# Performance work log

Measured on AMD Instinct MI355X. Metric: run time of the kernel, lower is better.

The kernel has to match this reference:

```python
import jax, jax.numpy as jnp
import numpy as np

N = 50000          # nodes
E = 1_600_000      # edges
H = 64             # agg_hidden (heads=1, concat)
IN = 7             # in_channels
EDIM = 4           # edge_dim
G = 256            # num graphs in batch
FC = 128           # fc_hidden
NC = 2             # num_classes
SLOPE = 0.2        # GATv2 LeakyReLU negative slope


def setup_inputs() -> dict:
    key = jax.random.key(0)
    ks = jax.random.split(key, 24)
    s = 0.1
    d = {
        "x": jax.random.normal(ks[0], (N, IN), dtype=jnp.float32),
        "edge_index": jax.random.randint(ks[1], (2, E), 0, N, dtype=jnp.int32),
        "edge_attr": jax.random.normal(ks[2], (E, EDIM), dtype=jnp.float32),
        "batch": jnp.sort(jax.random.randint(ks[3], (N,), 0, G, dtype=jnp.int32)),
        # GATv2 layer 0 (in=7 -> 64)
        "Wl0": jax.random.normal(ks[4], (IN, H)) * s,
        "bl0": jnp.zeros((H,), jnp.float32),
        "Wr0": jax.random.normal(ks[5], (IN, H)) * s,
        "br0": jnp.zeros((H,), jnp.float32),
        "We0": jax.random.normal(ks[6], (EDIM, H)) * s,
        "att0": jax.random.normal(ks[7], (H,)) * s,
        "bias0": jnp.zeros((H,), jnp.float32),
        # GATv2 layer 1 (64 -> 64)
        "Wl1": jax.random.normal(ks[8], (H, H)) * s,
        "bl1": jnp.zeros((H,), jnp.float32),
        "Wr1": jax.random.normal(ks[9], (H, H)) * s,
        "br1": jnp.zeros((H,), jnp.float32),
        "We1": jax.random.normal(ks[10], (EDIM, H)) * s,
        "att1": jax.random.normal(ks[11], (H,)) * s,
        "bias1": jnp.zeros((H,), jnp.float32),
        # MLP head
        "fc1_w": jax.random.normal(ks[12], (H, FC)) * s,
        "fc1_b": jnp.zeros((FC,), jnp.float32),
        "fc2_w": jax.random.normal(ks[13], (FC, NC)) * s,
        "fc2_b": jnp.zeros((NC,), jnp.float32),
    }
    return d


def _gatv2(x, src, dst, edge_attr, Wl, bl, Wr, br, We, att, bias):
    # GATv2Conv (heads=1, concat=True, edge_dim=EDIM), eval mode (no dropout)
    xl = x @ Wl + bl                         # source-side projection [N,H]
    xr = x @ Wr + br                         # target-side projection [N,H]
    e = xl[src] + xr[dst] + edge_attr @ We   # per-edge pre-activation [E,H]
    score = jax.nn.leaky_relu(e, SLOPE) @ att  # [E]
    # segment softmax over destination nodes
    m = jax.ops.segment_max(score, dst, num_segments=N)
    ex = jnp.exp(score - m[dst])
    den = jax.ops.segment_sum(ex, dst, num_segments=N)
    alpha = ex / (den[dst] + 1e-16)
    out = jax.ops.segment_sum(xl[src] * alpha[:, None], dst, num_segments=N)
    return out + bias


def reference(x, edge_index, edge_attr, batch,
              Wl0, bl0, Wr0, br0, We0, att0, bias0,
              Wl1, bl1, Wr1, br1, We1, att1, bias1,
              fc1_w, fc1_b, fc2_w, fc2_b):
    src, dst = edge_index[0], edge_index[1]
    h = jax.nn.elu(_gatv2(x, src, dst, edge_attr, Wl0, bl0, Wr0, br0, We0, att0, bias0))
    h = jax.nn.elu(_gatv2(h, src, dst, edge_attr, Wl1, bl1, Wr1, br1, We1, att1, bias1))
    # global mean pool over graphs
    sums = jax.ops.segment_sum(h, batch, num_segments=G)
    cnt = jax.ops.segment_sum(jnp.ones((h.shape[0],), h.dtype), batch, num_segments=G)
    g = sums / jnp.maximum(cnt, 1.0)[:, None]      # [G,H]
    g = jax.nn.relu(g @ fc1_w + fc1_b)
    logits = g @ fc2_w + fc2_b
    return jax.nn.log_softmax(logits, axis=1)
```

## Files before the change

kernel.cpp:

```cpp
#include <hip/hip_runtime.h>
#include <hip/hip_fp16.h>

#define N_NODES 50000
#define N_EDGES 1600000
#define H 64
#define IN_CH 7
#define EDIM 4
#define G_GRAPHS 256
#define FC 128
#define NC 2
#define SLOPE 0.2f
#define NBUCK 196
#define EPB1 8192
#define NB1 ((N_EDGES + EPB1 - 1) / EPB1)
#define PAIR_BLOCKS ((N_NODES * 32 + 255) / 256)

typedef _Float16 h2v __attribute__((ext_vector_type(2)));

__device__ __forceinline__ float fdot2f(h2v a, h2v b, float c) {
#if defined(__has_builtin) && __has_builtin(__builtin_amdgcn_fdot2)
    return __builtin_amdgcn_fdot2(a, b, c, false);
#else
    return c + (float)a[0] * (float)b[0] + (float)a[1] * (float)b[1];
#endif
}

__device__ __forceinline__ float wave_sum_to63(float x) {
    x += __int_as_float(__builtin_amdgcn_update_dpp(0, __float_as_int(x), 0x111, 0xf, 0xf, true));
    x += __int_as_float(__builtin_amdgcn_update_dpp(0, __float_as_int(x), 0x112, 0xf, 0xf, true));
    x += __int_as_float(__builtin_amdgcn_update_dpp(0, __float_as_int(x), 0x114, 0xf, 0xf, true));
    x += __int_as_float(__builtin_amdgcn_update_dpp(0, __float_as_int(x), 0x118, 0xf, 0xf, true));
    x += __int_as_float(__builtin_amdgcn_update_dpp(0, __float_as_int(x), 0x142, 0xf, 0xf, true));
    x += __int_as_float(__builtin_amdgcn_update_dpp(0, __float_as_int(x), 0x143, 0xf, 0xf, true));
    return x;
}
__device__ __forceinline__ float wave_max_to63(float x) {
    int xi = __float_as_int(x);
    x = fmaxf(x, __int_as_float(__builtin_amdgcn_update_dpp(xi, xi, 0x111, 0xf, 0xf, false))); xi = __float_as_int(x);
    x = fmaxf(x, __int_as_float(__builtin_amdgcn_update_dpp(xi, xi, 0x112, 0xf, 0xf, false))); xi = __float_as_int(x);
    x = fmaxf(x, __int_as_float(__builtin_amdgcn_update_dpp(xi, xi, 0x114, 0xf, 0xf, false))); xi = __float_as_int(x);
    x = fmaxf(x, __int_as_float(__builtin_amdgcn_update_dpp(xi, xi, 0x118, 0xf, 0xf, false))); xi = __float_as_int(x);
    x = fmaxf(x, __int_as_float(__builtin_amdgcn_update_dpp(xi, xi, 0x142, 0xf, 0xf, false))); xi = __float_as_int(x);
    x = fmaxf(x, __int_as_float(__builtin_amdgcn_update_dpp(xi, xi, 0x143, 0xf, 0xf, false)));
    return x;
}
__device__ __forceinline__ float lane63_bcast(float x) {
    return __int_as_float(__builtin_amdgcn_readlane(__float_as_int(x), 63));
}
__device__ __forceinline__ float readlane_f(float x, int i) {
    return __int_as_float(__builtin_amdgcn_readlane(__float_as_int(x), i));
}

__global__ __launch_bounds__(256) void front_kernel(
        const int* __restrict__ dst, int* __restrict__ rank1, int* __restrict__ bhist,
        const float* __restrict__ xin,
        const float* __restrict__ Wl0, const float* __restrict__ bl0,
        const float* __restrict__ Wr0, const float* __restrict__ br0,
        __half2* __restrict__ xlh, __half2* __restrict__ xrh,
        const float* __restrict__ We0, const float* __restrict__ We1,
        const float* __restrict__ Wl1, const float* __restrict__ bl1,
        const float* __restrict__ Wr1, const float* __restrict__ br1,
        __half2* __restrict__ weh0, __half2* __restrict__ weh1,
        __half2* __restrict__ wt, float* __restrict__ bb) {
    __shared__ int hist[NBUCK];
    int b = blockIdx.x;
    int t = threadIdx.x;
    if (b < NB1) {
        if (t < NBUCK) hist[t] = 0;
        __syncthreads();
#pragma unroll
        for (int i = 0; i < EPB1 / 256; ++i) {
            int e = b * EPB1 + i * 256 + t;
            if (e < N_EDGES) {
                int k = dst[e] >> 8;
                rank1[e] = atomicAdd(&hist[k], 1);
            }
        }
        __syncthreads();
        if (t < NBUCK) bhist[b * NBUCK + t] = hist[t];
    } else if (b < NB1 + PAIR_BLOCKS) {
        int idx = (b - NB1) * 256 + t;
        if (idx < N_NODES * 32) {
            int n = idx >> 5;
            int c = idx & 31;
            const float* xi = xin + n * IN_CH;
            float2 bl2 = ((const float2*)bl0)[c];
            float2 br2 = ((const float2*)br0)[c];
            float al0 = bl2.x, al1 = bl2.y, ar0 = br2.x, ar1 = br2.y;
#pragma unroll
            for (int k = 0; k < IN_CH; ++k) {
                float xv = xi[k];
                float2 wl2 = ((const float2*)(Wl0 + k * H))[c];
                float2 wr2 = ((const float2*)(Wr0 + k * H))[c];
                al0 += xv * wl2.x; al1 += xv * wl2.y;
                ar0 += xv * wr2.x; ar1 += xv * wr2.y;
            }
            xlh[idx] = __floats2half2_rn(al0, al1);
            xrh[idx] = __floats2half2_rn(ar0, ar1);
        }
    } else {
        if (t < 32) {
            for (int k = 0; k < 4; ++k)
                weh0[t * 4 + k] = __floats2half2_rn(We0[k * H + 2 * t], We0[k * H + 2 * t + 1]);
        } else if (t < 64) {
            int c = t - 32;
            for (int k = 0; k < 4; ++k)
                weh1[c * 4 + k] = __floats2half2_rn(We1[k * H + 2 * c], We1[k * H + 2 * c + 1]);
        }
        if (t < 128) {
            const float* W = (t < 64) ? Wl1 : Wr1;
            int c = t & 63;
            for (int kk = 0; kk < 32; ++kk)
                wt[t * 32 + kk] = __floats2half2_rn(W[(2 * kk) * H + c], W[(2 * kk + 1) * H + c]);
            bb[t] = (t < 64) ? bl1[c] : br1[c];
        }
    }
}

__global__ __launch_bounds__(256) void bucket_scan_kernel(
        const int* __restrict__ bhist, int* __restrict__ bases, int* __restrict__ cb_start) {
    __shared__ int lds[256];
    int t = threadIdx.x;
    int run = 0;
    if (t < NBUCK) {
        for (int b = 0; b < NB1; ++b) {
            bases[b * NBUCK + t] = run;
            run += bhist[b * NBUCK + t];
        }
    }
    lds[t] = (t < NBUCK) ? run : 0;
    __syncthreads();
    for (int off = 1; off < 256; off <<= 1) {
        int x = (t >= off) ? lds[t - off] : 0;
        __syncthreads();
        lds[t] += x;
        __syncthreads();
    }
    if (t < NBUCK) cb_start[t] = lds[t] - run;
    if (t == NBUCK - 1) cb_start[NBUCK] = lds[t];
}

__global__ void coarse_scatter_kernel(const int* __restrict__ src, const int* __restrict__ dst,
                                      const int* __restrict__ rank1, const int* __restrict__ bases,
                                      const int* __restrict__ cb_start,
                                      const float* __restrict__ edge_attr,
                                      int4* __restrict__ tmp) {
    int e = blockIdx.x * blockDim.x + threadIdx.x;
    if (e >= N_EDGES) return;
    int d = dst[e];
    int k = d >> 8;
    int b = e / EPB1;
    int slot = cb_start[k] + bases[b * NBUCK + k] + rank1[e];
    float4 ea = ((const float4*)edge_attr)[e];
    __half2 h01 = __floats2half2_rn(ea.x, ea.y);
    __half2 h23 = __floats2half2_rn(ea.z, ea.w);
    int4 ent;
    ent.x = src[e];
    ent.y = *reinterpret_cast<int*>(&h01);
    ent.z = *reinterpret_cast<int*>(&h23);
    ent.w = d;
    tmp[slot] = ent;
}

__global__ __launch_bounds__(256) void fine_sort_kernel(
        const int* __restrict__ cb_start, const int4* __restrict__ tmp,
        int4* __restrict__ csr, int* __restrict__ row_start) {
    __shared__ int hist2[256];
    __shared__ int cursor[256];
    __shared__ int lds[256];
    int k = blockIdx.x;
    int t = threadIdx.x;
    int beg = cb_start[k], end = cb_start[k + 1];
    hist2[t] = 0;
    __syncthreads();
    for (int i = beg + t; i < end; i += 256)
        atomicAdd(&hist2[tmp[i].w & 255], 1);
    __syncthreads();
    int v = hist2[t];
    lds[t] = v;
    __syncthreads();
    for (int off = 1; off < 256; off <<= 1) {
        int x = (t >= off) ? lds[t - off] : 0;
        __syncthreads();
        lds[t] += x;
        __syncthreads();
    }
    int pre = lds[t] - v;
    cursor[t] = pre;
    int node = k * 256 + t;
    if (node <= N_NODES) row_start[node] = beg + pre;
    if (k == NBUCK - 1 && t == 255 && N_NODES > node) row_start[N_NODES] = end;
    __syncthreads();
    for (int i = beg + t; i < end; i += 256) {
        int4 ent = tmp[i];
        int slot = beg + atomicAdd(&cursor[ent.w & 255], 1);
        csr[slot] = ent;
    }
}

__global__ __launch_bounds__(256) void proj1_kernel(
        const float* __restrict__ xin,
        const __half2* __restrict__ wt,
        const float* __restrict__ bb,
        __half2* __restrict__ xlh, __half2* __restrict__ xrh) {
    int g = __builtin_amdgcn_readfirstlane((int)(threadIdx.x >> 6));
    int lane = threadIdx.x & 63;
    int node = blockIdx.x * 64 + lane;
    if (node >= N_NODES) return;

    h2v xrow[32];
    const float4* xp = (const float4*)(xin + node * 64);
#pragma unroll
    for (int q = 0; q < 16; ++q) {
        float4 v = xp[q];
        __half2 a = __floats2half2_rn(v.x, v.y);
        __half2 b = __floats2half2_rn(v.z, v.w);
        xrow[2 * q]     = *reinterpret_cast<h2v*>(&a);
        xrow[2 * q + 1] = *reinterpret_cast<h2v*>(&b);
    }

    __half2* outp = (g < 2) ? xlh : xrh;
    int chbase = g * 32;
    int localbase = (g & 1) * 16;

#pragma unroll
    for (int cp = 0; cp < 16; ++cp) {
        int ch0 = chbase + 2 * cp;
        const h2v* w0 = (const h2v*)(wt + ch0 * 32);
        const h2v* w1 = (const h2v*)(wt + (ch0 + 1) * 32);
        float a0 = bb[ch0], a1 = bb[ch0 + 1];
#pragma unroll
        for (int kk = 0; kk < 32; ++kk) {
            a0 = fdot2f(xrow[kk], w0[kk], a0);
            a1 = fdot2f(xrow[kk], w1[kk], a1);
        }
        outp[node * 32 + localbase + cp] = __floats2half2_rn(a0, a1);
    }
}

__global__ __launch_bounds__(256) void score_kernel(
        const int4* __restrict__ csr,
        const __half2* __restrict__ xlh, const __half2* __restrict__ xrh,
        const __half2* __restrict__ weh, const float* __restrict__ att,
        float* __restrict__ score) {
    int e = blockIdx.x * blockDim.x + threadIdx.x;
    if (e >= N_EDGES) return;
    int4 ent = csr[e];
    __half2 ea01 = *reinterpret_cast<__half2*>(&ent.y);
    __half2 ea23 = *reinterpret_cast<__half2*>(&ent.z);
    __half2 e0 = __half2half2(__low2half(ea01));
    __half2 e1 = __half2half2(__high2half(ea01));
    __half2 e2 = __half2half2(__low2half(ea23));
    __half2 e3 = __half2half2(__high2half(ea23));
    const int4* xa = (const int4*)(xlh + ent.x * 32);
    const int4* xb = (const int4*)(xrh + ent.w * 32);
    float acc0 = 0.f, acc1 = 0.f;
#pragma unroll
    for (int k = 0; k < 8; ++k) {
        int4 va = xa[k];
        int4 vb = xb[k];
        const __half2* ha = reinterpret_cast<const __half2*>(&va);
        const __half2* hc = reinterpret_cast<const __half2*>(&vb);
#pragma unroll
        for (int j = 0; j < 4; ++j) {
            int c = k * 4 + j;
            __half2 v2 = __hadd2(ha[j], hc[j]);
            v2 = __hfma2(e0, weh[c * 4 + 0], v2);
            v2 = __hfma2(e1, weh[c * 4 + 1], v2);
            v2 = __hfma2(e2, weh[c * 4 + 2], v2);
            v2 = __hfma2(e3, weh[c * 4 + 3], v2);
            float2 vf = __half22float2(v2);
            float L0 = fmaxf(vf.x, SLOPE * vf.x);
            float L1 = fmaxf(vf.y, SLOPE * vf.y);
            float2 a2 = ((const float2*)att)[c];
            acc0 += L0 * a2.x;
            acc1 += L1 * a2.y;
        }
    }
    score[e] = acc0 + acc1;
}

__global__ __launch_bounds__(256) void agg_kernel(
        const int* __restrict__ row_start,
        const int4* __restrict__ csr,
        const float* __restrict__ score,
        const __half2* __restrict__ xlh,
        const float* __restrict__ bias,
        float* __restrict__ out) {
    int wave = (blockIdx.x * blockDim.x + threadIdx.x) >> 6;
    if (wave >= N_NODES) return;
    int lane = threadIdx.x & 63;
    int c = lane & 31;
    int hb = lane >> 5;
    int d = wave;
    int beg = __builtin_amdgcn_readfirstlane(row_start[d]);
    int end = __builtin_amdgcn_readfirstlane(row_start[d + 1]);

    float m = -INFINITY;
    for (int j = beg + lane; j < end; j += 64) m = fmaxf(m, score[j]);
    m = lane63_bcast(wave_max_to63(m));

    float l_lane = 0.f;
    float ax0 = 0.f, ay0 = 0.f, ax1 = 0.f, ay1 = 0.f;

    for (int cbeg = beg; cbeg < end; cbeg += 64) {
        int n = end - cbeg;
        int idx = cbeg + lane;
        float sc = score[min(idx, end - 1)];
        float p = __expf(sc - m);
        p = (lane < n) ? p : 0.f;
        l_lane += p;

        int nn = min(n, 64);
        int j = 0;
        for (; j + 4 <= nn; j += 4) {
            int sA0 = __builtin_amdgcn_readfirstlane(csr[cbeg + j + 0].x);
            int sB0 = __builtin_amdgcn_readfirstlane(csr[cbeg + j + 1].x);
            int sA1 = __builtin_amdgcn_readfirstlane(csr[cbeg + j + 2].x);
            int sB1 = __builtin_amdgcn_readfirstlane(csr[cbeg + j + 3].x);
            float pA0 = readlane_f(p, j + 0), pB0 = readlane_f(p, j + 1);
            float pA1 = readlane_f(p, j + 2), pB1 = readlane_f(p, j + 3);
            int s0 = hb ? sB0 : sA0;
            int s1 = hb ? sB1 : sA1;
            float pv0 = hb ? pB0 : pA0;
            float pv1 = hb ? pB1 : pA1;
            float2 x0 = __half22float2(xlh[s0 * 32 + c]);
            float2 x1 = __half22float2(xlh[s1 * 32 + c]);
            ax0 += pv0 * x0.x; ay0 += pv0 * x0.y;
            ax1 += pv1 * x1.x; ay1 += pv1 * x1.y;
        }
        for (; j + 2 <= nn; j += 2) {
            int sA = __builtin_amdgcn_readfirstlane(csr[cbeg + j + 0].x);
            int sB = __builtin_amdgcn_readfirstlane(csr[cbeg + j + 1].x);
            float pA = readlane_f(p, j + 0), pB = readlane_f(p, j + 1);
            int s = hb ? sB : sA;
            float pv = hb ? pB : pA;
            float2 xf = __half22float2(xlh[s * 32 + c]);
            ax0 += pv * xf.x; ay0 += pv * xf.y;
        }
        if (j < nn) {
            int sA = __builtin_amdgcn_readfirstlane(csr[cbeg + j].x);
            float pA = readlane_f(p, j);
            float pv = hb ? 0.f : pA;
            float2 xf = __half22float2(xlh[sA * 32 + c]);
            ax0 += pv * xf.x; ay0 += pv * xf.y;
        }
    }

    float l = lane63_bcast(wave_sum_to63(l_lane));
    float accx = ax0 + ax1, accy = ay0 + ay1;
    accx += __shfl_xor(accx, 32, 64);
    accy += __shfl_xor(accy, 32, 64);
    if (hb == 0) {
        float inv = 1.f / (l + 1e-16f);
        float2 b2 = ((const float2*)bias)[c];
        float o0 = accx * inv + b2.x;
        float o1 = accy * inv + b2.y;
        o0 = o0 > 0.f ? o0 : expm1f(o0);
        o1 = o1 > 0.f ? o1 : expm1f(o1);
        ((float2*)out)[d * 32 + c] = float2{o0, o1};
    }
}

__global__ __launch_bounds__(256) void pool_head_kernel(
        const float* __restrict__ h, const int* __restrict__ batch,
        const float* __restrict__ fc1w, const float* __restrict__ fc1b,
        const float* __restrict__ fc2w, const float* __restrict__ fc2b,
        float* __restrict__ out) {
    int g = blockIdx.x;
    int lo = 0, hi = N_NODES;
    while (lo < hi) { int mid = (lo + hi) >> 1; if (batch[mid] < g) lo = mid + 1; else hi = mid; }
    int start = lo;
    hi = N_NODES;
    while (lo < hi) { int mid = (lo + hi) >> 1; if (batch[mid] < g + 1) lo = mid + 1; else hi = mid; }
    int end = lo;

    int lane = threadIdx.x & 63;
    int w = threadIdx.x >> 6;
    float s = 0.f;
    for (int n = start + w; n < end; n += 4) s += h[n * H + lane];
    __shared__ float red[4][H];
    __shared__ float gv[H];
    __shared__ float f[FC];
    __shared__ float lg[NC];
    red[w][lane] = s;
    __syncthreads();
    if (w == 0) {
        float tot = red[0][lane] + red[1][lane] + red[2][lane] + red[3][lane];
        gv[lane] = tot / fmaxf((float)(end - start), 1.f);
    }
    __syncthreads();
    int t = threadIdx.x;
    if (t < FC) {
        float acc = fc1b[t];
#pragma unroll 16
        for (int k = 0; k < H; ++k) acc += gv[k] * fc1w[k * FC + t];
        f[t] = fmaxf(acc, 0.f);
    }
    __syncthreads();
    if (t < NC) {
        float a = fc2b[t];
        for (int k = 0; k < FC; ++k) a += f[k] * fc2w[k * NC + t];
        lg[t] = a;
    }
    __syncthreads();
    if (t < NC) {
        float mx = fmaxf(lg[0], lg[1]);
        float lse = mx + logf(expf(lg[0] - mx) + expf(lg[1] - mx));
        out[g * NC + t] = lg[t] - lse;
    }
}

extern "C" void kernel_launch(void* const* d_in, const int* in_sizes, int n_in,
                              void* d_out, int out_size, void* d_ws, size_t ws_size,
                              hipStream_t stream) {
    const float* x         = (const float*)d_in[0];
    const int*   edge_idx  = (const int*)d_in[1];
    const float* edge_attr = (const float*)d_in[2];
    const int*   batch     = (const int*)d_in[3];
    const float* Wl0  = (const float*)d_in[4];
    const float* bl0  = (const float*)d_in[5];
    const float* Wr0  = (const float*)d_in[6];
    const float* br0  = (const float*)d_in[7];
    const float* We0  = (const float*)d_in[8];
    const float* att0 = (const float*)d_in[9];
    const float* bias0= (const float*)d_in[10];
    const float* Wl1  = (const float*)d_in[11];
    const float* bl1  = (const float*)d_in[12];
    const float* Wr1  = (const float*)d_in[13];
    const float* br1  = (const float*)d_in[14];
    const float* We1  = (const float*)d_in[15];
    const float* att1 = (const float*)d_in[16];
    const float* bias1= (const float*)d_in[17];
    const float* fc1w = (const float*)d_in[18];
    const float* fc1b = (const float*)d_in[19];
    const float* fc2w = (const float*)d_in[20];
    const float* fc2b = (const float*)d_in[21];

    const int NH = N_NODES * H;
    __half2* xlh    = (__half2*)d_ws;
    __half2* xrh    = xlh + N_NODES * 32;
    float* C        = (float*)(xrh + N_NODES * 32);
    float* escore   = C + NH;
    float* pad      = escore + N_EDGES;
    int4*  tmp      = (int4*)C;
    int4*  csr      = (int4*)(pad + N_EDGES);
    int*   row_start= (int*)(csr + N_EDGES);
    int*   rank1    = row_start + N_NODES + 1;
    int*   bhist    = rank1 + N_EDGES;
    int*   bases    = bhist + NB1 * NBUCK;
    int*   cb_start = bases + NB1 * NBUCK;
    __half2* weh0   = (__half2*)(cb_start + NBUCK + 1);
    __half2* weh1   = weh0 + 128;
    __half2* wt1    = weh1 + 128;
    float* bb1      = (float*)(wt1 + 128 * 32);

    const int* src = edge_idx;
    const int* dst = edge_idx + N_EDGES;

    const int edgeBlocks = (N_EDGES + 255) / 256;
    const int waveBlocks = (N_NODES * 64 + 255) / 256;
    const int p1Blocks   = (N_NODES + 63) / 64;
    const int frontBlocks = NB1 + PAIR_BLOCKS + 1;

    front_kernel<<<frontBlocks, 256, 0, stream>>>(dst, rank1, bhist,
                                                  x, Wl0, bl0, Wr0, br0, xlh, xrh,
                                                  We0, We1, Wl1, bl1, Wr1, br1,
                                                  weh0, weh1, wt1, bb1);
    bucket_scan_kernel<<<1, 256, 0, stream>>>(bhist, bases, cb_start);
    coarse_scatter_kernel<<<edgeBlocks, 256, 0, stream>>>(src, dst, rank1, bases, cb_start,
                                                          edge_attr, tmp);
    fine_sort_kernel<<<NBUCK, 256, 0, stream>>>(cb_start, tmp, csr, row_start);

    score_kernel<<<edgeBlocks, 256, 0, stream>>>(csr, xlh, xrh, weh0, att0, escore);
    agg_kernel<<<waveBlocks, 256, 0, stream>>>(row_start, csr, escore, xlh, bias0, C);

    proj1_kernel<<<p1Blocks, 256, 0, stream>>>(C, wt1, bb1, xlh, xrh);
    score_kernel<<<edgeBlocks, 256, 0, stream>>>(csr, xlh, xrh, weh1, att1, escore);
    agg_kernel<<<waveBlocks, 256, 0, stream>>>(row_start, csr, escore, xlh, bias1, C);

    pool_head_kernel<<<G_GRAPHS, 256, 0, stream>>>(C, batch, fc1w, fc1b, fc2w, fc2b, (float*)d_out);
}
```

Before: 444.8 us.

## Fuse segment max into score kernel and use a compact source-index array

The score kernel now computes each destination's running max score. It does this with a block-local segmented max over the dst-sorted edges, then an atomicMax on an order-preserving unsigned encoding of the float. This removes the separate max pass over scores in the aggregation kernel. The sort also writes a packed int array of source indices, so aggregation reads 4 bytes per edge instead of a 16-byte CSR entry. The cost is extra shared-memory work and global atomics in the score kernel, plus resetting the max buffer in fine_sort and at the end of each aggregation.

```diff
diff --git a/kernel.cpp b/kernel.cpp
--- a/kernel.cpp
+++ b/kernel.cpp
@@ -25,6 +25,14 @@
 #endif
 }
 
+__device__ __forceinline__ unsigned enc_f(float f) {
+    unsigned b = __float_as_uint(f);
+    return (b & 0x80000000u) ? ~b : (b | 0x80000000u);
+}
+__device__ __forceinline__ float dec_f(unsigned u) {
+    return __uint_as_float((u & 0x80000000u) ? (u ^ 0x80000000u) : ~u);
+}
+
 __device__ __forceinline__ float wave_sum_to63(float x) {
     x += __int_as_float(__builtin_amdgcn_update_dpp(0, __float_as_int(x), 0x111, 0xf, 0xf, true));
     x += __int_as_float(__builtin_amdgcn_update_dpp(0, __float_as_int(x), 0x112, 0xf, 0xf, true));
@@ -32,16 +40,6 @@
     x += __int_as_float(__builtin_amdgcn_update_dpp(0, __float_as_int(x), 0x118, 0xf, 0xf, true));
     x += __int_as_float(__builtin_amdgcn_update_dpp(0, __float_as_int(x), 0x142, 0xf, 0xf, true));
     x += __int_as_float(__builtin_amdgcn_update_dpp(0, __float_as_int(x), 0x143, 0xf, 0xf, true));
-    return x;
-}
-__device__ __forceinline__ float wave_max_to63(float x) {
-    int xi = __float_as_int(x);
-    x = fmaxf(x, __int_as_float(__builtin_amdgcn_update_dpp(xi, xi, 0x111, 0xf, 0xf, false))); xi = __float_as_int(x);
-    x = fmaxf(x, __int_as_float(__builtin_amdgcn_update_dpp(xi, xi, 0x112, 0xf, 0xf, false))); xi = __float_as_int(x);
-    x = fmaxf(x, __int_as_float(__builtin_amdgcn_update_dpp(xi, xi, 0x114, 0xf, 0xf, false))); xi = __float_as_int(x);
-    x = fmaxf(x, __int_as_float(__builtin_amdgcn_update_dpp(xi, xi, 0x118, 0xf, 0xf, false))); xi = __float_as_int(x);
-    x = fmaxf(x, __int_as_float(__builtin_amdgcn_update_dpp(xi, xi, 0x142, 0xf, 0xf, false))); xi = __float_as_int(x);
-    x = fmaxf(x, __int_as_float(__builtin_amdgcn_update_dpp(xi, xi, 0x143, 0xf, 0xf, false)));
     return x;
 }
 __device__ __forceinline__ float lane63_bcast(float x) {
@@ -164,7 +162,8 @@
 
 __global__ __launch_bounds__(256) void fine_sort_kernel(
         const int* __restrict__ cb_start, const int4* __restrict__ tmp,
-        int4* __restrict__ csr, int* __restrict__ row_start) {
+        int4* __restrict__ csr, int* __restrict__ srcs,
+        int* __restrict__ row_start, unsigned* __restrict__ m_enc) {
     __shared__ int hist2[256];
     __shared__ int cursor[256];
     __shared__ int lds[256];
@@ -189,12 +188,13 @@
     cursor[t] = pre;
     int node = k * 256 + t;
     if (node <= N_NODES) row_start[node] = beg + pre;
-    if (k == NBUCK - 1 && t == 255 && N_NODES > node) row_start[N_NODES] = end;
+    if (node < N_NODES) m_enc[node] = 0u;
     __syncthreads();
     for (int i = beg + t; i < end; i += 256) {
         int4 ent = tmp[i];
         int slot = beg + atomicAdd(&cursor[ent.w & 255], 1);
         csr[slot] = ent;
+        srcs[slot] = ent.x;
     }
 }
 
@@ -242,9 +242,11 @@
         const int4* __restrict__ csr,
         const __half2* __restrict__ xlh, const __half2* __restrict__ xrh,
         const __half2* __restrict__ weh, const float* __restrict__ att,
-        float* __restrict__ score) {
-    int e = blockIdx.x * blockDim.x + threadIdx.x;
-    if (e >= N_EDGES) return;
+        float* __restrict__ score, unsigned* __restrict__ m_enc) {
+    __shared__ int sdst[256];
+    __shared__ float ssc[256];
+    int t = threadIdx.x;
+    int e = blockIdx.x * 256 + t;
     int4 ent = csr[e];
     __half2 ea01 = *reinterpret_cast<__half2*>(&ent.y);
     __half2 ea23 = *reinterpret_cast<__half2*>(&ent.z);
@@ -277,13 +279,24 @@
             acc1 += L1 * a2.y;
         }
     }
-    score[e] = acc0 + acc1;
+    float sc = acc0 + acc1;
+    score[e] = sc;
+    sdst[t] = ent.w;
+    ssc[t] = sc;
+    __syncthreads();
+    bool head = (t == 0) || (sdst[t] != sdst[t - 1]);
+    if (head) {
+        float mx = ssc[t];
+        for (int i = t + 1; i < 256 && sdst[i] == sdst[t]; ++i) mx = fmaxf(mx, ssc[i]);
+        atomicMax(&m_enc[sdst[t]], enc_f(mx));
+    }
 }
 
 __global__ __launch_bounds__(256) void agg_kernel(
         const int* __restrict__ row_start,
-        const int4* __restrict__ csr,
+        const int* __restrict__ srcs,
         const float* __restrict__ score,
+        unsigned* __restrict__ m_enc,
         const __half2* __restrict__ xlh,
         const float* __restrict__ bias,
         float* __restrict__ out) {
@@ -295,18 +308,14 @@
     int d = wave;
     int beg = __builtin_amdgcn_readfirstlane(row_start[d]);
     int end = __builtin_amdgcn_readfirstlane(row_start[d + 1]);
-
-    float m = -INFINITY;
-    for (int j = beg + lane; j < end; j += 64) m = fmaxf(m, score[j]);
-    m = lane63_bcast(wave_max_to63(m));
+    float m = dec_f(__builtin_amdgcn_readfirstlane(m_enc[d]));
 
     float l_lane = 0.f;
     float ax0 = 0.f, ay0 = 0.f, ax1 = 0.f, ay1 = 0.f;
 
     for (int cbeg = beg; cbeg < end; cbeg += 64) {
         int n = end - cbeg;
-        int idx = cbeg + lane;
-        float sc = score[min(idx, end - 1)];
+        float sc = score[cbeg + lane];
         float p = __expf(sc - m);
         p = (lane < n) ? p : 0.f;
         l_lane += p;
@@ -314,10 +323,10 @@
         int nn = min(n, 64);
         int j = 0;
         for (; j + 4 <= nn; j += 4) {
-            int sA0 = __builtin_amdgcn_readfirstlane(csr[cbeg + j + 0].x);
-            int sB0 = __builtin_amdgcn_readfirstlane(csr[cbeg + j + 1].x);
-            int sA1 = __builtin_amdgcn_readfirstlane(csr[cbeg + j + 2].x);
-            int sB1 = __builtin_amdgcn_readfirstlane(csr[cbeg + j + 3].x);
+            int sA0 = __builtin_amdgcn_readfirstlane(srcs[cbeg + j + 0]);
+            int sB0 = __builtin_amdgcn_readfirstlane(srcs[cbeg + j + 1]);
+            int sA1 = __builtin_amdgcn_readfirstlane(srcs[cbeg + j + 2]);
+            int sB1 = __builtin_amdgcn_readfirstlane(srcs[cbeg + j + 3]);
             float pA0 = readlane_f(p, j + 0), pB0 = readlane_f(p, j + 1);
             float pA1 = readlane_f(p, j + 2), pB1 = readlane_f(p, j + 3);
             int s0 = hb ? sB0 : sA0;
@@ -330,8 +339,8 @@
             ax1 += pv1 * x1.x; ay1 += pv1 * x1.y;
         }
         for (; j + 2 <= nn; j += 2) {
-            int sA = __builtin_amdgcn_readfirstlane(csr[cbeg + j + 0].x);
-            int sB = __builtin_amdgcn_readfirstlane(csr[cbeg + j + 1].x);
+            int sA = __builtin_amdgcn_readfirstlane(srcs[cbeg + j + 0]);
+            int sB = __builtin_amdgcn_readfirstlane(srcs[cbeg + j + 1]);
             float pA = readlane_f(p, j + 0), pB = readlane_f(p, j + 1);
             int s = hb ? sB : sA;
             float pv = hb ? pB : pA;
@@ -339,7 +348,7 @@
             ax0 += pv * xf.x; ay0 += pv * xf.y;
         }
         if (j < nn) {
-            int sA = __builtin_amdgcn_readfirstlane(csr[cbeg + j].x);
+            int sA = __builtin_amdgcn_readfirstlane(srcs[cbeg + j]);
             float pA = readlane_f(p, j);
             float pv = hb ? 0.f : pA;
             float2 xf = __half22float2(xlh[sA * 32 + c]);
@@ -359,6 +368,7 @@
         o0 = o0 > 0.f ? o0 : expm1f(o0);
         o1 = o1 > 0.f ? o1 : expm1f(o1);
         ((float2*)out)[d * 32 + c] = float2{o0, o1};
+        if (lane == 0) m_enc[d] = 0u;
     }
 }
 
@@ -445,8 +455,10 @@
     float* pad      = escore + N_EDGES;
     int4*  tmp      = (int4*)C;
     int4*  csr      = (int4*)(pad + N_EDGES);
-    int*   row_start= (int*)(csr + N_EDGES);
-    int*   rank1    = row_start + N_NODES + 1;
+    int*   srcs     = (int*)(csr + N_EDGES);
+    int*   row_start= srcs + N_EDGES;
+    unsigned* m_enc = (unsigned*)(row_start + N_NODES + 1);
+    int*   rank1    = (int*)(m_enc + N_NODES);
     int*   bhist    = rank1 + N_EDGES;
     int*   bases    = bhist + NB1 * NBUCK;
     int*   cb_start = bases + NB1 * NBUCK;
@@ -470,14 +482,14 @@
     bucket_scan_kernel<<<1, 256, 0, stream>>>(bhist, bases, cb_start);
     coarse_scatter_kernel<<<edgeBlocks, 256, 0, stream>>>(src, dst, rank1, bases, cb_start,
                                                           edge_attr, tmp);
-    fine_sort_kernel<<<NBUCK, 256, 0, stream>>>(cb_start, tmp, csr, row_start);
-
-    score_kernel<<<edgeBlocks, 256, 0, stream>>>(csr, xlh, xrh, weh0, att0, escore);
-    agg_kernel<<<waveBlocks, 256, 0, stream>>>(row_start, csr, escore, xlh, bias0, C);
+    fine_sort_kernel<<<NBUCK, 256, 0, stream>>>(cb_start, tmp, csr, srcs, row_start, m_enc);
+
+    score_kernel<<<edgeBlocks, 256, 0, stream>>>(csr, xlh, xrh, weh0, att0, escore, m_enc);
+    agg_kernel<<<waveBlocks, 256, 0, stream>>>(row_start, srcs, escore, m_enc, xlh, bias0, C);
 
     proj1_kernel<<<p1Blocks, 256, 0, stream>>>(C, wt1, bb1, xlh, xrh);
-    score_kernel<<<edgeBlocks, 256, 0, stream>>>(csr, xlh, xrh, weh1, att1, escore);
-    agg_kernel<<<waveBlocks, 256, 0, stream>>>(row_start, csr, escore, xlh, bias1, C);
+    score_kernel<<<edgeBlocks, 256, 0, stream>>>(csr, xlh, xrh, weh1, att1, escore, m_enc);
+    agg_kernel<<<waveBlocks, 256, 0, stream>>>(row_start, srcs, escore, m_enc, xlh, bias1, C);
 
     pool_head_kernel<<<G_GRAPHS, 256, 0, stream>>>(C, batch, fc1w, fc1b, fc2w, fc2b, (float*)d_out);
 }
```

Measured after the change: 435.0 us. -2.2%, faster.
